# Kernel optimization log

Measured on AMD Instinct MI355X. Metric: run time of the kernel, lower is better.

The kernel has to match this reference:

```python
import jax, jax.numpy as jnp
import numpy as np

B, H = 1_000_000, 18
TEMPERATURE = 1.0
EPS = 1e-8
NEG = -1e9  # stand-in for -inf that keeps logaddexp/exp finite


def setup_inputs() -> dict:
    key = jax.random.key(0)
    k1, k2, k3 = jax.random.split(key, 3)
    scores = jax.random.normal(k1, (B, H), dtype=jnp.float32)
    rankings = jax.random.randint(k2, (B, H), 0, 18, dtype=jnp.int32)
    mask = jax.random.randint(k3, (B, H), 0, 2, dtype=jnp.int32).astype(bool)
    return {"scores": scores, "rankings": rankings, "mask": mask}


def reference(scores, rankings, mask):
    # valid horses: masked-in and ranking >= 0
    valid = mask & (rankings >= 0)                      # (B, H) bool
    num_horses = scores.shape[1]

    # Stable sort valid horses to the front, ordered by ranking (Plackett-Luce order).
    sort_key = jnp.where(valid, rankings, num_horses + 1)
    order = jnp.argsort(sort_key, axis=1)               # stable
    s = jnp.take_along_axis(jnp.clip(scores, -10.0, 10.0), order, axis=1) / TEMPERATURE
    v = jnp.take_along_axis(valid, order, axis=1)
    s = jnp.where(v, s, NEG)                            # invalid horses contribute exp(-1e9)=0

    # Reverse cumulative logsumexp replaces the O(n^2) sequential softmax peel:
    # lse[i] = logsumexp(s[i:])  ->  log P(pick i-th) = s[i] - lse[i]
    lse = jax.lax.associative_scan(jnp.logaddexp, s, reverse=True, axis=1)
    prob = jnp.clip(jnp.exp(s - lse), EPS, 1.0 - EPS)   # matches original per-step prob clamp

    n = jnp.sum(valid, axis=1)                          # (B,) valid horse count
    # positions 0 .. n-2 contribute (last pick is deterministic)
    pos_ok = jnp.arange(num_horses)[None, :] < (n - 1)[:, None]
    race_loss = jnp.sum(jnp.where(pos_ok, -jnp.log(prob), 0.0), axis=1)

    race_valid = n >= 2                                 # races with <2 valid horses skipped
    num = jnp.sum(jnp.where(race_valid, race_loss, 0.0))
    den = jnp.sum(race_valid)
    return jnp.where(den > 0, num / jnp.maximum(den, 1).astype(num.dtype), jnp.float32(0.0))
```

## Files before the change

kernel.cpp:

```cpp
#include <hip/hip_runtime.h>
#include <stdint.h>

#define H 18
#define TPB 256
#define RPB 256

__global__ __launch_bounds__(TPB) void pl_main(const float* __restrict__ scores,
                                               const int* __restrict__ rankings,
                                               const unsigned char* __restrict__ mask8,
                                               int B,
                                               float* __restrict__ partial_loss,
                                               int* __restrict__ partial_cnt) {
    __shared__ float sMem[RPB * H];
    __shared__ unsigned short sKp[RPB * 9];
    __shared__ int sFlag;
    __shared__ float ls[TPB / 64];
    __shared__ int   cs[TPB / 64];

    const int t = threadIdx.x;
    const int lane = t & 63;
    const int wid = t >> 6;

    if (t == 0) sFlag = 0;
    __syncthreads();
    {
        unsigned int w = reinterpret_cast<const unsigned int*>(mask8)[t];
        if (__any(w > 1u) && lane == 0) atomicOr(&sFlag, 1);
    }
    __syncthreads();
    const bool u8mode = (sFlag != 0);

    const int race0 = blockIdx.x * RPB;
    const int limit = min(RPB, B - race0);
    const int nflat2 = limit * 9;

    const float2* g_s2 = reinterpret_cast<const float2*>(scores) + (size_t)race0 * 9;
    const int2*   g_r2 = reinterpret_cast<const int2*>(rankings) + (size_t)race0 * 9;
    float2* sS2 = reinterpret_cast<float2*>(sMem);

#pragma unroll
    for (int k = 0; k < 9; ++k) {
        int f2 = k * TPB + t;
        if (f2 < nflat2) {
            sS2[f2] = g_s2[f2];
            int2 rv = g_r2[f2];
            int m0, m1;
            if (u8mode) {
                uchar2 mb = *reinterpret_cast<const uchar2*>(
                    mask8 + (size_t)race0 * 18 + 2 * (size_t)f2);
                m0 = mb.x; m1 = mb.y;
            } else {
                int2 mb = reinterpret_cast<const int2*>(mask8)[(size_t)race0 * 9 + f2];
                m0 = mb.x; m1 = mb.y;
            }
            unsigned int k0 = (m0 != 0 && rv.x >= 0) ? (unsigned int)min(rv.x, 30) : 31u;
            unsigned int k1 = (m1 != 0 && rv.y >= 0) ? (unsigned int)min(rv.y, 30) : 31u;
            sKp[f2] = (unsigned short)(k0 | (k1 << 8));
        }
    }
    __syncthreads();

    float s[H];
    int key[H];
#pragma unroll
    for (int j = 0; j < H; ++j) key[j] = 31;
    float m = -1e30f;
    int n = 0;
    if (t < limit) {
#pragma unroll
        for (int j = 0; j < 9; ++j) {
            float2 sv = sS2[t * 9 + j];
            unsigned int kp = sKp[t * 9 + j];
            float s0 = fminf(fmaxf(sv.x, -10.0f), 10.0f);
            float s1 = fminf(fmaxf(sv.y, -10.0f), 10.0f);
            int k0 = (int)(kp & 0xffu);
            int k1 = (int)(kp >> 8);
            s[2 * j] = s0; s[2 * j + 1] = s1;
            key[2 * j] = k0; key[2 * j + 1] = k1;
            if (k0 < 31) { n++; m = fmaxf(m, s0); }
            if (k1 < 31) { n++; m = fmaxf(m, s1); }
        }
    }
    __syncthreads();

#pragma unroll
    for (int r = 0; r < H; ++r) sMem[r * RPB + t] = 0.0f;

#pragma unroll
    for (int j = 0; j < H; ++j) {
        if (key[j] < 31) {
            int a = key[j] * RPB + t;
            sMem[a] += __expf(s[j] - m);
        }
    }

    {
        float acc = 0.0f;
#pragma unroll
        for (int r = H - 1; r >= 0; --r) {
            acc += sMem[r * RPB + t];
            sMem[r * RPB + t] = acc;
        }
    }

    float th_loss = 0.0f;
    int th_cnt = 0;
    {
        float loss = 0.0f, last_term = 0.0f;
        int bk = -1;
#pragma unroll
        for (int j = 0; j < H; ++j) {
            if (key[j] < 31) {
                int a = key[j] * RPB + t;
                float run = sMem[a];
                float e = __expf(s[j] - m);
                sMem[a] = run - e;
                float term = m + __logf(run) - s[j];
                term = fminf(fmaxf(term, 1.0000000e-8f), 18.420680744f);
                loss += term;
                if (key[j] >= bk) { bk = key[j]; last_term = term; }
            }
        }
        if (n >= 2) { th_loss = loss - last_term; th_cnt = 1; }
    }

#pragma unroll
    for (int off = 32; off >= 1; off >>= 1) {
        th_loss += __shfl_down(th_loss, off);
        th_cnt  += __shfl_down(th_cnt, off);
    }
    if (lane == 0) { ls[wid] = th_loss; cs[wid] = th_cnt; }
    __syncthreads();
    if (t == 0) {
        float L = 0.0f; int C = 0;
#pragma unroll
        for (int w = 0; w < TPB / 64; ++w) { L += ls[w]; C += cs[w]; }
        partial_loss[blockIdx.x] = L;
        partial_cnt[blockIdx.x]  = C;
    }
}

__global__ __launch_bounds__(1024) void pl_final(const float* __restrict__ partial_loss,
                                                 const int* __restrict__ partial_cnt,
                                                 int nb, float* __restrict__ out) {
    float L = 0.0f;
    int C = 0;
    for (int i = threadIdx.x; i < nb; i += 1024) {
        L += partial_loss[i];
        C += partial_cnt[i];
    }
#pragma unroll
    for (int off = 32; off >= 1; off >>= 1) {
        L += __shfl_down(L, off);
        C += __shfl_down(C, off);
    }
    __shared__ float ls[1024 / 64];
    __shared__ int   cs[1024 / 64];
    int wid = threadIdx.x >> 6;
    int lane = threadIdx.x & 63;
    if (lane == 0) { ls[wid] = L; cs[wid] = C; }
    __syncthreads();
    if (threadIdx.x == 0) {
        float tl = 0.0f;
        int tc = 0;
#pragma unroll
        for (int w = 0; w < 1024 / 64; ++w) { tl += ls[w]; tc += cs[w]; }
        out[0] = (tc > 0) ? (tl / (float)tc) : 0.0f;
    }
}

extern "C" void kernel_launch(void* const* d_in, const int* in_sizes, int n_in,
                              void* d_out, int out_size, void* d_ws, size_t ws_size,
                              hipStream_t stream) {
    const float*         scores   = (const float*)d_in[0];
    const int*           rankings = (const int*)d_in[1];
    const unsigned char* mask     = (const unsigned char*)d_in[2];

    int B = in_sizes[0] / H;
    int nb = (B + RPB - 1) / RPB;

    float* pl = (float*)d_ws;
    int*   pc = (int*)((char*)d_ws + (((size_t)nb * sizeof(float) + 255) & ~(size_t)255));

    pl_main<<<nb, TPB, 0, stream>>>(scores, rankings, mask, B, pl, pc);
    pl_final<<<1, 1024, 0, stream>>>(pl, pc, nb, (float*)d_out);
}
```

Before: 225.8 us.

## Replace LDS histogram suffix-sum with register pairwise rank comparison

```diff
diff --git a/kernel.cpp b/kernel.cpp
--- a/kernel.cpp
+++ b/kernel.cpp
@@ -11,7 +11,7 @@
                                                int B,
                                                float* __restrict__ partial_loss,
                                                int* __restrict__ partial_cnt) {
-    __shared__ float sMem[RPB * H];
+    __shared__ float2 sS2[RPB * 9];
     __shared__ unsigned short sKp[RPB * 9];
     __shared__ int sFlag;
     __shared__ float ls[TPB / 64];
@@ -36,34 +36,58 @@
 
     const float2* g_s2 = reinterpret_cast<const float2*>(scores) + (size_t)race0 * 9;
     const int2*   g_r2 = reinterpret_cast<const int2*>(rankings) + (size_t)race0 * 9;
-    float2* sS2 = reinterpret_cast<float2*>(sMem);
-
-#pragma unroll
-    for (int k = 0; k < 9; ++k) {
-        int f2 = k * TPB + t;
-        if (f2 < nflat2) {
-            sS2[f2] = g_s2[f2];
-            int2 rv = g_r2[f2];
-            int m0, m1;
-            if (u8mode) {
+
+    if (blockIdx.x + 1 != (int)gridDim.x) {
+        if (u8mode) {
+#pragma unroll
+            for (int k = 0; k < 9; ++k) {
+                int f2 = k * TPB + t;
+                sS2[f2] = g_s2[f2];
+                int2 rv = g_r2[f2];
                 uchar2 mb = *reinterpret_cast<const uchar2*>(
                     mask8 + (size_t)race0 * 18 + 2 * (size_t)f2);
-                m0 = mb.x; m1 = mb.y;
-            } else {
+                unsigned int k0 = (mb.x != 0 && rv.x >= 0) ? (unsigned int)min(rv.x, 30) : 31u;
+                unsigned int k1 = (mb.y != 0 && rv.y >= 0) ? (unsigned int)min(rv.y, 30) : 31u;
+                sKp[f2] = (unsigned short)(k0 | (k1 << 8));
+            }
+        } else {
+#pragma unroll
+            for (int k = 0; k < 9; ++k) {
+                int f2 = k * TPB + t;
+                sS2[f2] = g_s2[f2];
+                int2 rv = g_r2[f2];
                 int2 mb = reinterpret_cast<const int2*>(mask8)[(size_t)race0 * 9 + f2];
-                m0 = mb.x; m1 = mb.y;
+                unsigned int k0 = (mb.x != 0 && rv.x >= 0) ? (unsigned int)min(rv.x, 30) : 31u;
+                unsigned int k1 = (mb.y != 0 && rv.y >= 0) ? (unsigned int)min(rv.y, 30) : 31u;
+                sKp[f2] = (unsigned short)(k0 | (k1 << 8));
             }
-            unsigned int k0 = (m0 != 0 && rv.x >= 0) ? (unsigned int)min(rv.x, 30) : 31u;
-            unsigned int k1 = (m1 != 0 && rv.y >= 0) ? (unsigned int)min(rv.y, 30) : 31u;
-            sKp[f2] = (unsigned short)(k0 | (k1 << 8));
+        }
+    } else {
+#pragma unroll
+        for (int k = 0; k < 9; ++k) {
+            int f2 = k * TPB + t;
+            if (f2 < nflat2) {
+                sS2[f2] = g_s2[f2];
+                int2 rv = g_r2[f2];
+                int m0, m1;
+                if (u8mode) {
+                    uchar2 mb = *reinterpret_cast<const uchar2*>(
+                        mask8 + (size_t)race0 * 18 + 2 * (size_t)f2);
+                    m0 = mb.x; m1 = mb.y;
+                } else {
+                    int2 mb = reinterpret_cast<const int2*>(mask8)[(size_t)race0 * 9 + f2];
+                    m0 = mb.x; m1 = mb.y;
+                }
+                unsigned int k0 = (m0 != 0 && rv.x >= 0) ? (unsigned int)min(rv.x, 30) : 31u;
+                unsigned int k1 = (m1 != 0 && rv.y >= 0) ? (unsigned int)min(rv.y, 30) : 31u;
+                sKp[f2] = (unsigned short)(k0 | (k1 << 8));
+            }
         }
     }
     __syncthreads();
 
     float s[H];
-    int key[H];
-#pragma unroll
-    for (int j = 0; j < H; ++j) key[j] = 31;
+    int ck[H];
     float m = -1e30f;
     int n = 0;
     if (t < limit) {
@@ -76,53 +100,52 @@
             int k0 = (int)(kp & 0xffu);
             int k1 = (int)(kp >> 8);
             s[2 * j] = s0; s[2 * j + 1] = s1;
-            key[2 * j] = k0; key[2 * j + 1] = k1;
-            if (k0 < 31) { n++; m = fmaxf(m, s0); }
-            if (k1 < 31) { n++; m = fmaxf(m, s1); }
-        }
-    }
-    __syncthreads();
-
-#pragma unroll
-    for (int r = 0; r < H; ++r) sMem[r * RPB + t] = 0.0f;
-
+            ck[2 * j]     = (k0 << 5) | (2 * j);
+            ck[2 * j + 1] = (k1 << 5) | (2 * j + 1);
+            bool v0 = k0 < 31, v1 = k1 < 31;
+            m = fmaxf(m, v0 ? s0 : -1e30f);
+            m = fmaxf(m, v1 ? s1 : -1e30f);
+            n += (v0 ? 1 : 0) + (v1 ? 1 : 0);
+        }
+    } else {
+#pragma unroll
+        for (int j = 0; j < H; ++j) { s[j] = 0.0f; ck[j] = (31 << 5) | j; }
+    }
+
+    float e[H];
 #pragma unroll
     for (int j = 0; j < H; ++j) {
-        if (key[j] < 31) {
-            int a = key[j] * RPB + t;
-            sMem[a] += __expf(s[j] - m);
-        }
-    }
-
-    {
-        float acc = 0.0f;
-#pragma unroll
-        for (int r = H - 1; r >= 0; --r) {
-            acc += sMem[r * RPB + t];
-            sMem[r * RPB + t] = acc;
-        }
-    }
-
-    float th_loss = 0.0f;
-    int th_cnt = 0;
-    {
-        float loss = 0.0f, last_term = 0.0f;
-        int bk = -1;
-#pragma unroll
-        for (int j = 0; j < H; ++j) {
-            if (key[j] < 31) {
-                int a = key[j] * RPB + t;
-                float run = sMem[a];
-                float e = __expf(s[j] - m);
-                sMem[a] = run - e;
-                float term = m + __logf(run) - s[j];
-                term = fminf(fmaxf(term, 1.0000000e-8f), 18.420680744f);
-                loss += term;
-                if (key[j] >= bk) { bk = key[j]; last_term = term; }
-            }
-        }
-        if (n >= 2) { th_loss = loss - last_term; th_cnt = 1; }
-    }
+        e[j] = (ck[j] < (31 << 5)) ? __expf(s[j] - m) : 0.0f;
+    }
+
+    float run[H];
+#pragma unroll
+    for (int a = 0; a < H; ++a) run[a] = e[a];
+#pragma unroll
+    for (int a = 0; a < H; ++a) {
+#pragma unroll
+        for (int b = a + 1; b < H; ++b) {
+            bool cc = ck[b] > ck[a];
+            run[a] += cc ? e[b] : 0.0f;
+            run[b] += cc ? 0.0f : e[a];
+        }
+    }
+
+    float loss = 0.0f, last_term = 0.0f;
+    int best = -1;
+#pragma unroll
+    for (int j = 0; j < H; ++j) {
+        float term = m + __logf(run[j]) - s[j];
+        term = fminf(fmaxf(term, 1.0000000e-8f), 18.420680744f);
+        bool v = ck[j] < (31 << 5);
+        loss += v ? term : 0.0f;
+        int ckv = v ? ck[j] : -1;
+        bool up = ckv > best;
+        best = up ? ckv : best;
+        last_term = up ? term : last_term;
+    }
+    float th_loss = (n >= 2) ? (loss - last_term) : 0.0f;
+    int th_cnt = (n >= 2) ? 1 : 0;
 
 #pragma unroll
     for (int off = 32; off >= 1; off >>= 1) {
```

Measured after the change: 213.0 us. 1.06x faster.

## Split each race across two threads with pairwise rank-comparison suffix sums

Applied to the files above, without the earlier changes.

```diff
diff --git a/kernel.cpp b/kernel.cpp
--- a/kernel.cpp
+++ b/kernel.cpp
@@ -3,7 +3,7 @@
 
 #define H 18
 #define TPB 256
-#define RPB 256
+#define RPB 128
 
 __global__ __launch_bounds__(TPB) void pl_main(const float* __restrict__ scores,
                                                const int* __restrict__ rankings,
@@ -11,8 +11,8 @@
                                                int B,
                                                float* __restrict__ partial_loss,
                                                int* __restrict__ partial_cnt) {
-    __shared__ float sMem[RPB * H];
-    __shared__ unsigned short sKp[RPB * 9];
+    __shared__ float sS[RPB * H];
+    __shared__ unsigned char sK8[RPB * H];
     __shared__ int sFlag;
     __shared__ float ls[TPB / 64];
     __shared__ int   cs[TPB / 64];
@@ -36,14 +36,13 @@
 
     const float2* g_s2 = reinterpret_cast<const float2*>(scores) + (size_t)race0 * 9;
     const int2*   g_r2 = reinterpret_cast<const int2*>(rankings) + (size_t)race0 * 9;
-    float2* sS2 = reinterpret_cast<float2*>(sMem);
 
 #pragma unroll
-    for (int k = 0; k < 9; ++k) {
+    for (int k = 0; k < 5; ++k) {
         int f2 = k * TPB + t;
         if (f2 < nflat2) {
-            sS2[f2] = g_s2[f2];
-            int2 rv = g_r2[f2];
+            float2 sv = g_s2[f2];
+            int2   rv = g_r2[f2];
             int m0, m1;
             if (u8mode) {
                 uchar2 mb = *reinterpret_cast<const uchar2*>(
@@ -53,76 +52,77 @@
                 int2 mb = reinterpret_cast<const int2*>(mask8)[(size_t)race0 * 9 + f2];
                 m0 = mb.x; m1 = mb.y;
             }
+            float s0 = fminf(fmaxf(sv.x, -10.0f), 10.0f);
+            float s1 = fminf(fmaxf(sv.y, -10.0f), 10.0f);
+            reinterpret_cast<float2*>(sS)[f2] = make_float2(s0, s1);
             unsigned int k0 = (m0 != 0 && rv.x >= 0) ? (unsigned int)min(rv.x, 30) : 31u;
             unsigned int k1 = (m1 != 0 && rv.y >= 0) ? (unsigned int)min(rv.y, 30) : 31u;
-            sKp[f2] = (unsigned short)(k0 | (k1 << 8));
+            reinterpret_cast<unsigned short*>(sK8)[f2] = (unsigned short)(k0 | (k1 << 8));
         }
     }
     __syncthreads();
 
-    float s[H];
-    int key[H];
+    const int rb  = t >> 1;
+    const int sub = t & 1;
+    const bool live = rb < limit;
+
+    float s[9], e[9], run[9];
+    int ck[9];
+    int nloc = 0;
 #pragma unroll
-    for (int j = 0; j < H; ++j) key[j] = 31;
-    float m = -1e30f;
-    int n = 0;
-    if (t < limit) {
+    for (int i = 0; i < 9; ++i) {
+        int j = sub * 9 + i;
+        float sv = sS[rb * H + j];
+        int kk = live ? (int)sK8[rb * H + j] : 31;
+        bool v = kk < 31;
+        s[i] = sv;
+        ck[i] = (kk << 5) | j;
+        e[i] = v ? __expf(sv) : 0.0f;
+        nloc += v ? 1 : 0;
+    }
+
 #pragma unroll
-        for (int j = 0; j < 9; ++j) {
-            float2 sv = sS2[t * 9 + j];
-            unsigned int kp = sKp[t * 9 + j];
-            float s0 = fminf(fmaxf(sv.x, -10.0f), 10.0f);
-            float s1 = fminf(fmaxf(sv.y, -10.0f), 10.0f);
-            int k0 = (int)(kp & 0xffu);
-            int k1 = (int)(kp >> 8);
-            s[2 * j] = s0; s[2 * j + 1] = s1;
-            key[2 * j] = k0; key[2 * j + 1] = k1;
-            if (k0 < 31) { n++; m = fmaxf(m, s0); }
-            if (k1 < 31) { n++; m = fmaxf(m, s1); }
+    for (int i = 0; i < 9; ++i) run[i] = e[i];
+#pragma unroll
+    for (int a = 0; a < 9; ++a) {
+#pragma unroll
+        for (int b = a + 1; b < 9; ++b) {
+            bool cc = ck[b] > ck[a];
+            run[a] += cc ? e[b] : 0.0f;
+            run[b] += cc ? 0.0f : e[a];
         }
     }
-    __syncthreads();
-
 #pragma unroll
-    for (int r = 0; r < H; ++r) sMem[r * RPB + t] = 0.0f;
-
+    for (int p = 0; p < 9; ++p) {
+        float pe = __shfl_xor(e[p], 1);
+        int  pck = __shfl_xor(ck[p], 1);
 #pragma unroll
-    for (int j = 0; j < H; ++j) {
-        if (key[j] < 31) {
-            int a = key[j] * RPB + t;
-            sMem[a] += __expf(s[j] - m);
+        for (int i = 0; i < 9; ++i) {
+            run[i] += (pck > ck[i]) ? pe : 0.0f;
         }
     }
 
-    {
-        float acc = 0.0f;
+    float loss = 0.0f, last = 0.0f;
+    int best = -1;
 #pragma unroll
-        for (int r = H - 1; r >= 0; --r) {
-            acc += sMem[r * RPB + t];
-            sMem[r * RPB + t] = acc;
-        }
+    for (int i = 0; i < 9; ++i) {
+        float term = __logf(run[i]) - s[i];
+        term = fminf(fmaxf(term, 1.0000000e-8f), 18.420680744f);
+        bool v = ck[i] < (31 << 5);
+        loss += v ? term : 0.0f;
+        int c = v ? ck[i] : -1;
+        bool up = c > best;
+        best = up ? c : best;
+        last = up ? term : last;
     }
 
-    float th_loss = 0.0f;
-    int th_cnt = 0;
-    {
-        float loss = 0.0f, last_term = 0.0f;
-        int bk = -1;
-#pragma unroll
-        for (int j = 0; j < H; ++j) {
-            if (key[j] < 31) {
-                int a = key[j] * RPB + t;
-                float run = sMem[a];
-                float e = __expf(s[j] - m);
-                sMem[a] = run - e;
-                float term = m + __logf(run) - s[j];
-                term = fminf(fmaxf(term, 1.0000000e-8f), 18.420680744f);
-                loss += term;
-                if (key[j] >= bk) { bk = key[j]; last_term = term; }
-            }
-        }
-        if (n >= 2) { th_loss = loss - last_term; th_cnt = 1; }
-    }
+    loss += __shfl_xor(loss, 1);
+    int n = nloc + __shfl_xor(nloc, 1);
+    int pbest = __shfl_xor(best, 1);
+    float plast = __shfl_xor(last, 1);
+    last = (pbest > best) ? plast : last;
+    float th_loss = (n >= 2 && sub == 0) ? (loss - last) : 0.0f;
+    int th_cnt = (n >= 2 && sub == 0) ? 1 : 0;
 
 #pragma unroll
     for (int off = 32; off >= 1; off >>= 1) {
```

New measurement: 214.8 us. -4.8%, faster.
